# Optimization experiments

Hardware: AMD Instinct MI355X
Metric: run time of the kernel (lower is better)

Reference implementation:

```python
import jax, jax.numpy as jnp
import numpy as np

N_EMBD = 1024
N_HEAD = 16
HEAD_DIM = N_EMBD // N_HEAD


def setup_inputs() -> dict:
    key = jax.random.key(0)
    ks = jax.random.split(key, 9)
    B, T, C = 4, 2048, N_EMBD
    s = 1.0 / np.sqrt(C)
    return {
        "x": jax.random.normal(ks[0], (B, T, C), dtype=jnp.float32),
        "Wk": jax.random.normal(ks[1], (C, C), dtype=jnp.float32) * s,
        "bk": jax.random.normal(ks[2], (C,), dtype=jnp.float32) * 0.02,
        "Wq": jax.random.normal(ks[3], (C, C), dtype=jnp.float32) * s,
        "bq": jax.random.normal(ks[4], (C,), dtype=jnp.float32) * 0.02,
        "Wv": jax.random.normal(ks[5], (C, C), dtype=jnp.float32) * s,
        "bv": jax.random.normal(ks[6], (C,), dtype=jnp.float32) * 0.02,
        "Wp": jax.random.normal(ks[7], (C, C), dtype=jnp.float32) * s,
        "bp": jax.random.normal(ks[8], (C,), dtype=jnp.float32) * 0.02,
    }


def reference(x, Wk, bk, Wq, bq, Wv, bv, Wp, bp):
    B, T, C = x.shape
    nh, hs = N_HEAD, HEAD_DIM
    # linear projections; weights stored as [in, out] (x @ W + b)
    k = (x @ Wk + bk).reshape(B, T, nh, hs).transpose(0, 2, 1, 3)  # [B,nh,T,hs]
    q = (x @ Wq + bq).reshape(B, T, nh, hs).transpose(0, 2, 1, 3)
    v = (x @ Wv + bv).reshape(B, T, nh, hs).transpose(0, 2, 1, 3)
    att = jnp.einsum("bhqd,bhkd->bhqk", q, k) / jnp.sqrt(jnp.float32(hs))
    causal = jnp.tril(jnp.ones((T, T), dtype=bool))  # [T,T]
    att = jnp.where(causal[None, None], att, -jnp.inf)
    att = jax.nn.softmax(att, axis=-1)
    y = jnp.einsum("bhqk,bhkd->bhqd", att, v)  # [B,nh,T,hs]
    y = y.transpose(0, 2, 1, 3).reshape(B, T, C)
    return y @ Wp + bp
```

## Files before the change

kernel.cpp:

```cpp
#include <hip/hip_runtime.h>

#define TSEQ 2048
#define CDIM 1024
#define NH 16
#define HS 64
#define BATCH 4

typedef __attribute__((ext_vector_type(8))) short short8;
typedef __attribute__((ext_vector_type(4))) short s16x4;
typedef __attribute__((ext_vector_type(4))) float f32x4;

__device__ __forceinline__ short f2bf(float f) {
    unsigned u = __builtin_bit_cast(unsigned, f);
    unsigned r = (u + 0x7fffu + ((u >> 16) & 1u)) >> 16;
    return (short)r;
}

__device__ __forceinline__ void gload_lds16(const void* g, void* l) {
    __builtin_amdgcn_global_load_lds((const __attribute__((address_space(1))) void*)g,
                                     (__attribute__((address_space(3))) void*)l, 16, 0, 0);
}

#define FENCE() asm volatile("" ::: "memory")

__global__ void prep(const float* __restrict__ x, short* __restrict__ xb,
                     const float* __restrict__ Wk, const float* __restrict__ Wq,
                     const float* __restrict__ Wv, const float* __restrict__ Wp,
                     short* __restrict__ Wcat, short* __restrict__ Wpt) {
    __shared__ float tl[64][65];
    const int bid = blockIdx.x, t = threadIdx.x;
    if (bid < 8192) {
        int i = bid * 256 + t;
        float4 v = ((const float4*)x)[i];
        s16x4 r;
        r[0] = f2bf(v.x); r[1] = f2bf(v.y); r[2] = f2bf(v.z); r[3] = f2bf(v.w);
        ((s16x4*)xb)[i] = r;
        return;
    }
    const int widx = bid - 8192;
    const int z = widx >> 8, rem = widx & 255;
    const int k0 = (rem & 15) * 64, n0 = (rem >> 4) * 64;
    const float* src; short* dst;
    if (z == 0)      { src = Wq; dst = Wcat; }
    else if (z == 1) { src = Wk; dst = Wcat + 1048576; }
    else if (z == 2) { src = Wv; dst = Wcat + 2097152; }
    else             { src = Wp; dst = Wpt; }
    const int tx = t & 63, ty = t >> 6;
#pragma unroll
    for (int i = 0; i < 16; ++i) {
        int r = i * 4 + ty;
        tl[r][tx] = src[(size_t)(k0 + r) * CDIM + n0 + tx];
    }
    __syncthreads();
#pragma unroll
    for (int i = 0; i < 16; ++i) {
        int r = i * 4 + ty;
        dst[(size_t)(n0 + r) * CDIM + k0 + tx] = f2bf(tl[tx][r]);
    }
}

__global__ __launch_bounds__(512, 4) void gemm96(const short* __restrict__ A,
                                                 const short* __restrict__ Bt,
                                                 const float* __restrict__ bq,
                                                 const float* __restrict__ bk,
                                                 const float* __restrict__ bv,
                                                 float alphaQ,
                                                 short* __restrict__ C,
                                                 short* __restrict__ Vt) {
    __shared__ short As[256 * 64];
    __shared__ short Bs[96 * 64];
    const int t = threadIdx.x;
    const int lane = t & 63, w = t >> 6;
    const int lr = lane & 15, lg = lane >> 4;
    const int wr = w >> 1, wc = w & 1;
    const int tl = (blockIdx.x & 7) * 128 + (blockIdx.x >> 3);
    const int mbase = (tl >> 5) * 256, nbase = (tl & 31) * 96;
    f32x4 acc[4][3] = {};
    for (int k0 = 0; k0 < 1024; k0 += 64) {
#pragma unroll
        for (int i = 0; i < 4; ++i) {
            int chunk = i * 512 + t;
            int r = chunk >> 3, c = chunk & 7;
            int cl = c ^ (r & 7);
            gload_lds16(A + (size_t)(mbase + r) * 1024 + k0 + cl * 8, As + chunk * 8);
        }
        {
            int r = t >> 3, c = t & 7;
            int cl = c ^ (r & 7);
            gload_lds16(Bt + (size_t)(nbase + r) * 1024 + k0 + cl * 8, Bs + t * 8);
            if (t < 256) {
                int chunk = 512 + t;
                int r2 = chunk >> 3, c2 = chunk & 7;
                int cl2 = c2 ^ (r2 & 7);
                gload_lds16(Bt + (size_t)(nbase + r2) * 1024 + k0 + cl2 * 8, Bs + chunk * 8);
            }
        }
        __syncthreads();
#pragma unroll
        for (int ks = 0; ks < 2; ++ks) {
            short8 a[4], b[3];
#pragma unroll
            for (int mi = 0; mi < 4; ++mi) {
                int row = wr * 64 + mi * 16 + lr;
                int ch = (ks * 4 + lg) ^ (row & 7);
                a[mi] = *(const short8*)(As + row * 64 + ch * 8);
            }
#pragma unroll
            for (int ni = 0; ni < 3; ++ni) {
                int row = wc * 48 + ni * 16 + lr;
                int ch = (ks * 4 + lg) ^ (row & 7);
                b[ni] = *(const short8*)(Bs + row * 64 + ch * 8);
            }
#pragma unroll
            for (int mi = 0; mi < 4; ++mi)
#pragma unroll
                for (int ni = 0; ni < 3; ++ni)
                    acc[mi][ni] = __builtin_amdgcn_mfma_f32_16x16x32_bf16(a[mi], b[ni],
                                                                          acc[mi][ni], 0, 0, 0);
        }
        __syncthreads();
    }
    const int btok = mbase & (TSEQ - 1);
    const int bidx = mbase >> 11;
#pragma unroll
    for (int mi = 0; mi < 4; ++mi) {
#pragma unroll
        for (int ni = 0; ni < 3; ++ni) {
            const int col = nbase + wc * 48 + ni * 16 + lr;
            const float bvv = (col < 1024) ? bq[col]
                            : (col < 2048) ? bk[col - 1024] : bv[col - 2048];
            if (col >= 2048) {
                const int dfull = col - 2048;
                const int tok0 = btok + wr * 64 + mi * 16 + lg * 4;
                s16x4 pk;
#pragma unroll
                for (int ii = 0; ii < 4; ++ii) pk[ii] = f2bf(acc[mi][ni][ii] + bvv);
                *(s16x4*)(Vt + (size_t)(bidx * 1024 + dfull) * TSEQ + tok0) = pk;
            } else {
                const float alpha = (col < 1024) ? alphaQ : 1.0f;
#pragma unroll
                for (int ii = 0; ii < 4; ++ii) {
                    const int row = mbase + wr * 64 + mi * 16 + lg * 4 + ii;
                    C[(size_t)row * 3072 + col] = f2bf((acc[mi][ni][ii] + bvv) * alpha);
                }
            }
        }
    }
}

__global__ __launch_bounds__(256) void gemm_bt(const short* __restrict__ A,
                                               const short* __restrict__ Bt,
                                               const float* __restrict__ bias,
                                               float* __restrict__ Cout) {
    __shared__ short As[128 * 64];
    __shared__ short Bs[128 * 64];
    const int t = threadIdx.x;
    const int lane = t & 63, w = t >> 6;
    const int lr = lane & 15, lg = lane >> 4;
    const int wr = w >> 1, wc = w & 1;
    const int mbase = blockIdx.y * 128, nbase = blockIdx.x * 128;
    f32x4 acc[4][4] = {};
    for (int k0 = 0; k0 < 1024; k0 += 64) {
#pragma unroll
        for (int i = 0; i < 4; ++i) {
            int chunk = i * 256 + t;
            int r = chunk >> 3, c = chunk & 7;
            int cl = c ^ (r & 7);
            gload_lds16(A + (size_t)(mbase + r) * 1024 + k0 + cl * 8, As + chunk * 8);
            gload_lds16(Bt + (size_t)(nbase + r) * 1024 + k0 + cl * 8, Bs + chunk * 8);
        }
        __syncthreads();
#pragma unroll
        for (int ks = 0; ks < 2; ++ks) {
            short8 a[4], b[4];
#pragma unroll
            for (int mi = 0; mi < 4; ++mi) {
                int row = wr * 64 + mi * 16 + lr;
                int ch = (ks * 4 + lg) ^ (row & 7);
                a[mi] = *(const short8*)(As + row * 64 + ch * 8);
            }
#pragma unroll
            for (int ni = 0; ni < 4; ++ni) {
                int row = wc * 64 + ni * 16 + lr;
                int ch = (ks * 4 + lg) ^ (row & 7);
                b[ni] = *(const short8*)(Bs + row * 64 + ch * 8);
            }
#pragma unroll
            for (int mi = 0; mi < 4; ++mi)
#pragma unroll
                for (int ni = 0; ni < 4; ++ni)
                    acc[mi][ni] = __builtin_amdgcn_mfma_f32_16x16x32_bf16(a[mi], b[ni],
                                                                          acc[mi][ni], 0, 0, 0);
        }
        __syncthreads();
    }
#pragma unroll
    for (int mi = 0; mi < 4; ++mi) {
#pragma unroll
        for (int ni = 0; ni < 4; ++ni) {
            int col = nbase + wc * 64 + ni * 16 + lr;
            float bvv = bias[col];
#pragma unroll
            for (int i = 0; i < 4; ++i) {
                int row = mbase + wr * 64 + mi * 16 + lg * 4 + i;
                Cout[(size_t)row * 1024 + col] = acc[mi][ni][i] + bvv;
            }
        }
    }
}

__global__ __launch_bounds__(512, 3) void attn(const short* __restrict__ QKV,
                                               const short* __restrict__ Vt,
                                               short* __restrict__ Y) {
    __shared__ short Kl[2][64 * 64];
    __shared__ short Vl[2][64 * 64];
    __shared__ short Pl[8][16 * 64];
    const int t = threadIdx.x, lane = t & 63, w = t >> 6;
    const int lr = lane & 15, lg = lane >> 4;
    const int bid = blockIdx.x;
    const int cx = bid & 7, sx = bid >> 3;
    const int bh = cx * 8 + (sx >> 3), pb = sx & 7;
    const int b = bh >> 4, h = bh & 15;
    const size_t rowbase = (size_t)b * TSEQ;
    const float SHIFT2 = 17.31234049f;
    const int sr = t >> 3, sc = t & 7, scl = sc ^ (sr & 7);
    const short* Kg = QKV + 1024 + h * HS;

#define STAGE(bf, j0n) do { \
    gload_lds16(Kg + (rowbase + (j0n) + sr) * 3072 + scl * 8, &Kl[bf][t * 8]); \
    gload_lds16(Vt + (size_t)(bh * 64 + sr) * TSEQ + (j0n) + scl * 8, &Vl[bf][t * 8]); \
} while (0)

    const int useg0 = 15 - pb, useg1 = pb;
    for (int sg = 0; sg < 2; ++sg) {
        const int u = sg ? useg1 : useg0;
        const int q0w = u * 128 + w * 16;
        const int niter = 2 * u + 2;
        short8 qf[2];
#pragma unroll
        for (int ks = 0; ks < 2; ++ks)
            qf[ks] = *(const short8*)(QKV + (rowbase + q0w + lr) * 3072 + h * HS +
                                      ks * 32 + lg * 8);
        float l_i[4] = {0.f, 0.f, 0.f, 0.f};
        f32x4 o[4] = {};
        STAGE(0, 0);
        int buf = 0;
        for (int jt = 0; jt < niter; ++jt) {
            const int j0 = jt * 64;
            if (jt + 1 < niter) {
                STAGE(buf ^ 1, j0 + 64);
                asm volatile("s_waitcnt vmcnt(2)" ::: "memory");
            } else {
                asm volatile("s_waitcnt vmcnt(0)" ::: "memory");
            }
            __builtin_amdgcn_s_barrier();
            FENCE();
            if (j0 <= q0w + 15) {
                f32x4 s[4];
                __builtin_amdgcn_s_setprio(1);
#pragma unroll
                for (int nt = 0; nt < 4; ++nt) {
                    s[nt] = f32x4{-SHIFT2, -SHIFT2, -SHIFT2, -SHIFT2};
                    if (j0 + nt * 16 <= q0w + 15) {
#pragma unroll
                        for (int ks = 0; ks < 2; ++ks) {
                            short8 kf = *(const short8*)(&Kl[buf][(nt * 16 + lr) * 64 +
                                                        (((ks * 4 + lg) ^ (lr & 7)) * 8)]);
                            s[nt] = __builtin_amdgcn_mfma_f32_16x16x32_bf16(qf[ks], kf,
                                                                            s[nt], 0, 0, 0);
                        }
                    }
                }
                __builtin_amdgcn_s_setprio(0);
                if (j0 + 63 > q0w) {
#pragma unroll
                    for (int nt = 0; nt < 4; ++nt)
#pragma unroll
                        for (int i = 0; i < 4; ++i) {
                            int kv = j0 + nt * 16 + lr;
                            int q = q0w + lg * 4 + i;
                            if (kv > q) s[nt][i] = -__builtin_inff();
                        }
                }
#pragma unroll
                for (int i = 0; i < 4; ++i) {
                    const int ql = lg * 4 + i;
                    float pt[4];
#pragma unroll
                    for (int nt = 0; nt < 4; ++nt) {
                        float p = __builtin_amdgcn_exp2f(s[nt][i]);
                        unsigned uu = __builtin_bit_cast(unsigned, p);
                        int chv = ((nt * 2 + (lr >> 3)) ^ (ql & 7));
                        Pl[w][ql * 64 + chv * 8 + (lr & 7)] = (short)(uu >> 16);
                        pt[nt] = p;
                    }
                    l_i[i] += (pt[0] + pt[1]) + (pt[2] + pt[3]);
                }
                short8 pf[2];
#pragma unroll
                for (int ks = 0; ks < 2; ++ks)
                    pf[ks] = *(const short8*)(&Pl[w][lr * 64 +
                                                     (((ks * 4 + lg) ^ (lr & 7)) * 8)]);
                __builtin_amdgcn_s_setprio(1);
#pragma unroll
                for (int nd = 0; nd < 4; ++nd)
#pragma unroll
                    for (int ks = 0; ks < 2; ++ks) {
                        short8 vf = *(const short8*)(&Vl[buf][(nd * 16 + lr) * 64 +
                                                    (((ks * 4 + lg) ^ (lr & 7)) * 8)]);
                        o[nd] = __builtin_amdgcn_mfma_f32_16x16x32_bf16(pf[ks], vf,
                                                                        o[nd], 0, 0, 0);
                    }
                __builtin_amdgcn_s_setprio(0);
            }
            FENCE();
            __builtin_amdgcn_s_barrier();
            buf ^= 1;
        }
#pragma unroll
        for (int i = 0; i < 4; ++i) {
            float l = l_i[i];
            l += __shfl_xor(l, 1);
            l += __shfl_xor(l, 2);
            l += __shfl_xor(l, 4);
            l += __shfl_xor(l, 8);
            float inv = 1.0f / l;
            int q = q0w + lg * 4 + i;
#pragma unroll
            for (int nd = 0; nd < 4; ++nd)
                Y[(rowbase + q) * 1024 + h * HS + nd * 16 + lr] = f2bf(o[nd][i] * inv);
        }
        __syncthreads();
    }
#undef STAGE
}

extern "C" void kernel_launch(void* const* d_in, const int* in_sizes, int n_in,
                              void* d_out, int out_size, void* d_ws, size_t ws_size,
                              hipStream_t stream) {
    const float* x  = (const float*)d_in[0];
    const float* Wk = (const float*)d_in[1];
    const float* bk = (const float*)d_in[2];
    const float* Wq = (const float*)d_in[3];
    const float* bq = (const float*)d_in[4];
    const float* Wv = (const float*)d_in[5];
    const float* bv = (const float*)d_in[6];
    const float* Wp = (const float*)d_in[7];
    const float* bp = (const float*)d_in[8];
    float* out = (float*)d_out;
    char* ws = (char*)d_ws;
    const size_t MB = 1024 * 1024;
    short* xb   = (short*)(ws);
    short* Wcat = (short*)(ws + 16 * MB);
    short* Wpt  = (short*)(ws + 22 * MB);
    short* QKVb = (short*)(ws + 24 * MB);
    short* Yb   = xb;
    short* VtT  = (short*)d_out;

    const float alphaQ = 0.125f * 1.44269504088896f;

    prep<<<9216, 256, 0, stream>>>(x, xb, Wk, Wq, Wv, Wp, Wcat, Wpt);
    gemm96<<<1024, 512, 0, stream>>>(xb, Wcat, bq, bk, bv, alphaQ, QKVb, VtT);
    attn<<<512, 512, 0, stream>>>(QKVb, VtT, Yb);
    gemm_bt<<<dim3(8, 64), 256, 0, stream>>>(Yb, Wpt, bp, out);
}
```

Measured before the change: 160.6 us.

## Share K/V tile loads across paired causal query segments in attention

```diff
diff --git a/kernel.cpp b/kernel.cpp
--- a/kernel.cpp
+++ b/kernel.cpp
@@ -209,7 +209,7 @@
     }
 }
 
-__global__ __launch_bounds__(512, 3) void attn(const short* __restrict__ QKV,
+__global__ __launch_bounds__(512, 4) void attn(const short* __restrict__ QKV,
                                                const short* __restrict__ Vt,
                                                short* __restrict__ Y) {
     __shared__ short Kl[2][64 * 64];
@@ -231,108 +231,118 @@
     gload_lds16(Vt + (size_t)(bh * 64 + sr) * TSEQ + (j0n) + scl * 8, &Vl[bf][t * 8]); \
 } while (0)
 
-    const int useg0 = 15 - pb, useg1 = pb;
-    for (int sg = 0; sg < 2; ++sg) {
-        const int u = sg ? useg1 : useg0;
-        const int q0w = u * 128 + w * 16;
-        const int niter = 2 * u + 2;
-        short8 qf[2];
-#pragma unroll
-        for (int ks = 0; ks < 2; ++ks)
-            qf[ks] = *(const short8*)(QKV + (rowbase + q0w + lr) * 3072 + h * HS +
-                                      ks * 32 + lg * 8);
-        float l_i[4] = {0.f, 0.f, 0.f, 0.f};
-        f32x4 o[4] = {};
-        STAGE(0, 0);
-        int buf = 0;
-        for (int jt = 0; jt < niter; ++jt) {
-            const int j0 = jt * 64;
-            if (jt + 1 < niter) {
-                STAGE(buf ^ 1, j0 + 64);
-                asm volatile("s_waitcnt vmcnt(2)" ::: "memory");
-            } else {
-                asm volatile("s_waitcnt vmcnt(0)" ::: "memory");
-            }
-            __builtin_amdgcn_s_barrier();
-            FENCE();
-            if (j0 <= q0w + 15) {
-                f32x4 s[4];
-                __builtin_amdgcn_s_setprio(1);
-#pragma unroll
-                for (int nt = 0; nt < 4; ++nt) {
-                    s[nt] = f32x4{-SHIFT2, -SHIFT2, -SHIFT2, -SHIFT2};
-                    if (j0 + nt * 16 <= q0w + 15) {
-#pragma unroll
-                        for (int ks = 0; ks < 2; ++ks) {
-                            short8 kf = *(const short8*)(&Kl[buf][(nt * 16 + lr) * 64 +
-                                                        (((ks * 4 + lg) ^ (lr & 7)) * 8)]);
-                            s[nt] = __builtin_amdgcn_mfma_f32_16x16x32_bf16(qf[ks], kf,
-                                                                            s[nt], 0, 0, 0);
-                        }
-                    }
-                }
-                __builtin_amdgcn_s_setprio(0);
-                if (j0 + 63 > q0w) {
-#pragma unroll
-                    for (int nt = 0; nt < 4; ++nt)
-#pragma unroll
-                        for (int i = 0; i < 4; ++i) {
-                            int kv = j0 + nt * 16 + lr;
-                            int q = q0w + lg * 4 + i;
-                            if (kv > q) s[nt][i] = -__builtin_inff();
-                        }
-                }
-#pragma unroll
-                for (int i = 0; i < 4; ++i) {
-                    const int ql = lg * 4 + i;
-                    float pt[4];
-#pragma unroll
-                    for (int nt = 0; nt < 4; ++nt) {
-                        float p = __builtin_amdgcn_exp2f(s[nt][i]);
-                        unsigned uu = __builtin_bit_cast(unsigned, p);
-                        int chv = ((nt * 2 + (lr >> 3)) ^ (ql & 7));
-                        Pl[w][ql * 64 + chv * 8 + (lr & 7)] = (short)(uu >> 16);
-                        pt[nt] = p;
-                    }
-                    l_i[i] += (pt[0] + pt[1]) + (pt[2] + pt[3]);
-                }
-                short8 pf[2];
-#pragma unroll
-                for (int ks = 0; ks < 2; ++ks)
-                    pf[ks] = *(const short8*)(&Pl[w][lr * 64 +
-                                                     (((ks * 4 + lg) ^ (lr & 7)) * 8)]);
-                __builtin_amdgcn_s_setprio(1);
-#pragma unroll
-                for (int nd = 0; nd < 4; ++nd)
-#pragma unroll
-                    for (int ks = 0; ks < 2; ++ks) {
-                        short8 vf = *(const short8*)(&Vl[buf][(nd * 16 + lr) * 64 +
-                                                    (((ks * 4 + lg) ^ (lr & 7)) * 8)]);
-                        o[nd] = __builtin_amdgcn_mfma_f32_16x16x32_bf16(pf[ks], vf,
-                                                                        o[nd], 0, 0, 0);
-                    }
-                __builtin_amdgcn_s_setprio(0);
-            }
-            FENCE();
-            __builtin_amdgcn_s_barrier();
-            buf ^= 1;
-        }
-#pragma unroll
-        for (int i = 0; i < 4; ++i) {
-            float l = l_i[i];
-            l += __shfl_xor(l, 1);
-            l += __shfl_xor(l, 2);
-            l += __shfl_xor(l, 4);
-            l += __shfl_xor(l, 8);
-            float inv = 1.0f / l;
-            int q = q0w + lg * 4 + i;
-#pragma unroll
-            for (int nd = 0; nd < 4; ++nd)
-                Y[(rowbase + q) * 1024 + h * HS + nd * 16 + lr] = f2bf(o[nd][i] * inv);
-        }
-        __syncthreads();
-    }
+#define UNIT_BODY(qf_, l_, o_, q0w_) do { \
+    if (j0 <= (q0w_) + 15) { \
+        f32x4 s[4]; \
+        __builtin_amdgcn_s_setprio(1); \
+        _Pragma("unroll") \
+        for (int nt = 0; nt < 4; ++nt) { \
+            s[nt] = f32x4{-SHIFT2, -SHIFT2, -SHIFT2, -SHIFT2}; \
+            if (j0 + nt * 16 <= (q0w_) + 15) { \
+                _Pragma("unroll") \
+                for (int ks = 0; ks < 2; ++ks) { \
+                    short8 kf = *(const short8*)(&Kl[buf][(nt * 16 + lr) * 64 + \
+                                                 (((ks * 4 + lg) ^ (lr & 7)) * 8)]); \
+                    s[nt] = __builtin_amdgcn_mfma_f32_16x16x32_bf16(qf_[ks], kf, \
+                                                                    s[nt], 0, 0, 0); \
+                } \
+            } \
+        } \
+        __builtin_amdgcn_s_setprio(0); \
+        if (j0 + 63 > (q0w_)) { \
+            _Pragma("unroll") \
+            for (int nt = 0; nt < 4; ++nt) \
+                _Pragma("unroll") \
+                for (int i = 0; i < 4; ++i) { \
+                    int kv = j0 + nt * 16 + lr; \
+                    int q = (q0w_) + lg * 4 + i; \
+                    if (kv > q) s[nt][i] = -__builtin_inff(); \
+                } \
+        } \
+        _Pragma("unroll") \
+        for (int i = 0; i < 4; ++i) { \
+            const int ql = lg * 4 + i; \
+            float pt[4]; \
+            _Pragma("unroll") \
+            for (int nt = 0; nt < 4; ++nt) { \
+                float p = __builtin_amdgcn_exp2f(s[nt][i]); \
+                unsigned uu = __builtin_bit_cast(unsigned, p); \
+                int chv = ((nt * 2 + (lr >> 3)) ^ (ql & 7)); \
+                Pl[w][ql * 64 + chv * 8 + (lr & 7)] = (short)(uu >> 16); \
+                pt[nt] = p; \
+            } \
+            l_[i] += (pt[0] + pt[1]) + (pt[2] + pt[3]); \
+        } \
+        short8 pf[2]; \
+        _Pragma("unroll") \
+        for (int ks = 0; ks < 2; ++ks) \
+            pf[ks] = *(const short8*)(&Pl[w][lr * 64 + (((ks * 4 + lg) ^ (lr & 7)) * 8)]); \
+        __builtin_amdgcn_s_setprio(1); \
+        _Pragma("unroll") \
+        for (int nd = 0; nd < 4; ++nd) \
+            _Pragma("unroll") \
+            for (int ks = 0; ks < 2; ++ks) { \
+                short8 vf = *(const short8*)(&Vl[buf][(nd * 16 + lr) * 64 + \
+                                             (((ks * 4 + lg) ^ (lr & 7)) * 8)]); \
+                o_[nd] = __builtin_amdgcn_mfma_f32_16x16x32_bf16(pf[ks], vf, \
+                                                                 o_[nd], 0, 0, 0); \
+            } \
+        __builtin_amdgcn_s_setprio(0); \
+    } \
+} while (0)
+
+#define UNIT_EPI(l_, o_, q0w_) do { \
+    _Pragma("unroll") \
+    for (int i = 0; i < 4; ++i) { \
+        float l = l_[i]; \
+        l += __shfl_xor(l, 1); \
+        l += __shfl_xor(l, 2); \
+        l += __shfl_xor(l, 4); \
+        l += __shfl_xor(l, 8); \
+        float inv = 1.0f / l; \
+        int q = (q0w_) + lg * 4 + i; \
+        _Pragma("unroll") \
+        for (int nd = 0; nd < 4; ++nd) \
+            Y[(rowbase + q) * 1024 + h * HS + nd * 16 + lr] = f2bf(o_[nd][i] * inv); \
+    } \
+} while (0)
+
+    const int uA = 15 - pb, uB = pb;
+    const int q0wA = uA * 128 + w * 16, q0wB = uB * 128 + w * 16;
+    const int niterA = 2 * uA + 2;
+    short8 qfA[2], qfB[2];
+#pragma unroll
+    for (int ks = 0; ks < 2; ++ks) {
+        qfA[ks] = *(const short8*)(QKV + (rowbase + q0wA + lr) * 3072 + h * HS +
+                                   ks * 32 + lg * 8);
+        qfB[ks] = *(const short8*)(QKV + (rowbase + q0wB + lr) * 3072 + h * HS +
+                                   ks * 32 + lg * 8);
+    }
+    float lA[4] = {0.f, 0.f, 0.f, 0.f}, lB[4] = {0.f, 0.f, 0.f, 0.f};
+    f32x4 oA[4] = {}, oB[4] = {};
+    STAGE(0, 0);
+    int buf = 0;
+    for (int jt = 0; jt < niterA; ++jt) {
+        const int j0 = jt * 64;
+        if (jt + 1 < niterA) {
+            STAGE(buf ^ 1, j0 + 64);
+            asm volatile("s_waitcnt vmcnt(2)" ::: "memory");
+        } else {
+            asm volatile("s_waitcnt vmcnt(0)" ::: "memory");
+        }
+        __builtin_amdgcn_s_barrier();
+        FENCE();
+        UNIT_BODY(qfA, lA, oA, q0wA);
+        UNIT_BODY(qfB, lB, oB, q0wB);
+        FENCE();
+        __builtin_amdgcn_s_barrier();
+        buf ^= 1;
+    }
+    UNIT_EPI(lA, oA, q0wA);
+    UNIT_EPI(lB, oB, q0wB);
 #undef STAGE
+#undef UNIT_BODY
+#undef UNIT_EPI
 }
 
 extern "C" void kernel_launch(void* const* d_in, const int* in_sizes, int n_in,
```

Result: slower. 164.6 us (+2.4%).

## Stage 128-key KV tiles per barrier in causal attention kernel

Applied to the files above, without the earlier changes.

```diff
diff --git a/kernel.cpp b/kernel.cpp
--- a/kernel.cpp
+++ b/kernel.cpp
@@ -209,11 +209,11 @@
     }
 }
 
-__global__ __launch_bounds__(512, 3) void attn(const short* __restrict__ QKV,
+__global__ __launch_bounds__(512, 2) void attn(const short* __restrict__ QKV,
                                                const short* __restrict__ Vt,
                                                short* __restrict__ Y) {
-    __shared__ short Kl[2][64 * 64];
-    __shared__ short Vl[2][64 * 64];
+    __shared__ short Kl[2][128 * 64];
+    __shared__ short Vl[2][64 * 128];
     __shared__ short Pl[8][16 * 64];
     const int t = threadIdx.x, lane = t & 63, w = t >> 6;
     const int lr = lane & 15, lg = lane >> 4;
@@ -223,19 +223,25 @@
     const int b = bh >> 4, h = bh & 15;
     const size_t rowbase = (size_t)b * TSEQ;
     const float SHIFT2 = 17.31234049f;
-    const int sr = t >> 3, sc = t & 7, scl = sc ^ (sr & 7);
+    const int krA = t >> 3, krB = 64 + (t >> 3);
+    const int kcl = (t & 7) ^ (krA & 7);
+    const int vrA = t >> 4, vrB = 32 + (t >> 4);
+    const int vclA = (t & 15) ^ (vrA & 7);
     const short* Kg = QKV + 1024 + h * HS;
 
 #define STAGE(bf, j0n) do { \
-    gload_lds16(Kg + (rowbase + (j0n) + sr) * 3072 + scl * 8, &Kl[bf][t * 8]); \
-    gload_lds16(Vt + (size_t)(bh * 64 + sr) * TSEQ + (j0n) + scl * 8, &Vl[bf][t * 8]); \
+    gload_lds16(Kg + (rowbase + (j0n) + krA) * 3072 + kcl * 8, &Kl[bf][t * 8]); \
+    gload_lds16(Kg + (rowbase + (j0n) + krB) * 3072 + kcl * 8, &Kl[bf][(512 + t) * 8]); \
+    gload_lds16(Vt + (size_t)(bh * 64 + vrA) * TSEQ + (j0n) + vclA * 8, &Vl[bf][t * 8]); \
+    gload_lds16(Vt + (size_t)(bh * 64 + vrB) * TSEQ + (j0n) + vclA * 8, \
+                &Vl[bf][(512 + t) * 8]); \
 } while (0)
 
     const int useg0 = 15 - pb, useg1 = pb;
     for (int sg = 0; sg < 2; ++sg) {
         const int u = sg ? useg1 : useg0;
         const int q0w = u * 128 + w * 16;
-        const int niter = 2 * u + 2;
+        const int niter = u + 1;
         short8 qf[2];
 #pragma unroll
         for (int ks = 0; ks < 2; ++ks)
@@ -246,72 +252,77 @@
         STAGE(0, 0);
         int buf = 0;
         for (int jt = 0; jt < niter; ++jt) {
-            const int j0 = jt * 64;
             if (jt + 1 < niter) {
-                STAGE(buf ^ 1, j0 + 64);
-                asm volatile("s_waitcnt vmcnt(2)" ::: "memory");
+                STAGE(buf ^ 1, (jt + 1) * 128);
+                asm volatile("s_waitcnt vmcnt(4)" ::: "memory");
             } else {
                 asm volatile("s_waitcnt vmcnt(0)" ::: "memory");
             }
             __builtin_amdgcn_s_barrier();
             FENCE();
-            if (j0 <= q0w + 15) {
-                f32x4 s[4];
-                __builtin_amdgcn_s_setprio(1);
-#pragma unroll
-                for (int nt = 0; nt < 4; ++nt) {
-                    s[nt] = f32x4{-SHIFT2, -SHIFT2, -SHIFT2, -SHIFT2};
-                    if (j0 + nt * 16 <= q0w + 15) {
-#pragma unroll
-                        for (int ks = 0; ks < 2; ++ks) {
-                            short8 kf = *(const short8*)(&Kl[buf][(nt * 16 + lr) * 64 +
-                                                        (((ks * 4 + lg) ^ (lr & 7)) * 8)]);
-                            s[nt] = __builtin_amdgcn_mfma_f32_16x16x32_bf16(qf[ks], kf,
-                                                                            s[nt], 0, 0, 0);
+#pragma unroll
+            for (int hf = 0; hf < 2; ++hf) {
+                const int j0 = jt * 128 + hf * 64;
+                if (j0 <= q0w + 15) {
+                    f32x4 s[4];
+                    __builtin_amdgcn_s_setprio(1);
+#pragma unroll
+                    for (int nt = 0; nt < 4; ++nt) {
+                        s[nt] = f32x4{-SHIFT2, -SHIFT2, -SHIFT2, -SHIFT2};
+                        if (j0 + nt * 16 <= q0w + 15) {
+                            const int kr = hf * 64 + nt * 16 + lr;
+#pragma unroll
+                            for (int ks = 0; ks < 2; ++ks) {
+                                short8 kf = *(const short8*)(&Kl[buf][kr * 64 +
+                                                    (((ks * 4 + lg) ^ (kr & 7)) * 8)]);
+                                s[nt] = __builtin_amdgcn_mfma_f32_16x16x32_bf16(
+                                    qf[ks], kf, s[nt], 0, 0, 0);
+                            }
                         }
                     }
+                    __builtin_amdgcn_s_setprio(0);
+                    if (j0 + 63 > q0w) {
+#pragma unroll
+                        for (int nt = 0; nt < 4; ++nt)
+#pragma unroll
+                            for (int i = 0; i < 4; ++i) {
+                                int kv = j0 + nt * 16 + lr;
+                                int q = q0w + lg * 4 + i;
+                                if (kv > q) s[nt][i] = -__builtin_inff();
+                            }
+                    }
+#pragma unroll
+                    for (int i = 0; i < 4; ++i) {
+                        const int ql = lg * 4 + i;
+                        float pt[4];
+#pragma unroll
+                        for (int nt = 0; nt < 4; ++nt) {
+                            float p = __builtin_amdgcn_exp2f(s[nt][i]);
+                            unsigned uu = __builtin_bit_cast(unsigned, p);
+                            int chv = ((nt * 2 + (lr >> 3)) ^ (ql & 7));
+                            Pl[w][ql * 64 + chv * 8 + (lr & 7)] = (short)(uu >> 16);
+                            pt[nt] = p;
+                        }
+                        l_i[i] += (pt[0] + pt[1]) + (pt[2] + pt[3]);
+                    }
+                    short8 pf[2];
+#pragma unroll
+                    for (int ks = 0; ks < 2; ++ks)
+                        pf[ks] = *(const short8*)(&Pl[w][lr * 64 +
+                                                  (((ks * 4 + lg) ^ (lr & 7)) * 8)]);
+                    __builtin_amdgcn_s_setprio(1);
+#pragma unroll
+                    for (int nd = 0; nd < 4; ++nd)
+#pragma unroll
+                        for (int ks = 0; ks < 2; ++ks) {
+                            const int vr = nd * 16 + lr;
+                            const int vc = (hf * 8 + ks * 4 + lg) ^ (vr & 7);
+                            short8 vf = *(const short8*)(&Vl[buf][vr * 128 + vc * 8]);
+                            o[nd] = __builtin_amdgcn_mfma_f32_16x16x32_bf16(
+                                pf[ks], vf, o[nd], 0, 0, 0);
+                        }
+                    __builtin_amdgcn_s_setprio(0);
                 }
-                __builtin_amdgcn_s_setprio(0);
-                if (j0 + 63 > q0w) {
-#pragma unroll
-                    for (int nt = 0; nt < 4; ++nt)
-#pragma unroll
-                        for (int i = 0; i < 4; ++i) {
-                            int kv = j0 + nt * 16 + lr;
-                            int q = q0w + lg * 4 + i;
-                            if (kv > q) s[nt][i] = -__builtin_inff();
-                        }
-                }
-#pragma unroll
-                for (int i = 0; i < 4; ++i) {
-                    const int ql = lg * 4 + i;
-                    float pt[4];
-#pragma unroll
-                    for (int nt = 0; nt < 4; ++nt) {
-                        float p = __builtin_amdgcn_exp2f(s[nt][i]);
-                        unsigned uu = __builtin_bit_cast(unsigned, p);
-                        int chv = ((nt * 2 + (lr >> 3)) ^ (ql & 7));
-                        Pl[w][ql * 64 + chv * 8 + (lr & 7)] = (short)(uu >> 16);
-                        pt[nt] = p;
-                    }
-                    l_i[i] += (pt[0] + pt[1]) + (pt[2] + pt[3]);
-                }
-                short8 pf[2];
-#pragma unroll
-                for (int ks = 0; ks < 2; ++ks)
-                    pf[ks] = *(const short8*)(&Pl[w][lr * 64 +
-                                                     (((ks * 4 + lg) ^ (lr & 7)) * 8)]);
-                __builtin_amdgcn_s_setprio(1);
-#pragma unroll
-                for (int nd = 0; nd < 4; ++nd)
-#pragma unroll
-                    for (int ks = 0; ks < 2; ++ks) {
-                        short8 vf = *(const short8*)(&Vl[buf][(nd * 16 + lr) * 64 +
-                                                    (((ks * 4 + lg) ^ (lr & 7)) * 8)]);
-                        o[nd] = __builtin_amdgcn_mfma_f32_16x16x32_bf16(pf[ks], vf,
-                                                                        o[nd], 0, 0, 0);
-                    }
-                __builtin_amdgcn_s_setprio(0);
             }
             FENCE();
             __builtin_amdgcn_s_barrier();
```

Result: slower. 180.3 us (+12.2%).
